# Performance work log

Measured on AMD Instinct MI355X. Metric: run time of the kernel, lower is better.

The kernel has to match this reference:

```python
import jax, jax.numpy as jnp
import numpy as np

MASK_NUM = float(-2**32 + 1)  # additive masking constant from the original module


def setup_inputs() -> dict:
    key = jax.random.key(0)
    kq, kk, kv, km = jax.random.split(key, 4)
    BH, S, D = 32, 2048, 64   # batch*heads, seq_len, head_dim
    B = 4                     # true batch (masks leading dim)
    queries = jax.random.normal(kq, (BH, S, D), dtype=jnp.float32)
    keys = jax.random.normal(kk, (BH, S, D), dtype=jnp.float32)
    values = jax.random.normal(kv, (BH, S, D), dtype=jnp.float32)
    masks = jax.random.randint(km, (B, S), 0, 2, dtype=jnp.int32)  # 1 = masked key
    return {"queries": queries, "keys": keys, "values": values, "masks": masks}


def reference(queries, keys, values, masks):
    d = queries.shape[-1]
    # QK^T, scaled by sqrt(d): [BH, Sq, Sk]
    scores = jnp.einsum('bqd,bkd->bqk', queries, keys) / (d ** 0.5)
    # key-padding mask: tile [B, Sk] -> [BH, Sk], additive large negative
    heads = queries.shape[0] // masks.shape[0]
    m = jnp.tile(masks.astype(jnp.float32), (heads, 1))[:, None, :]  # [BH,1,Sk]
    scores = scores + m * MASK_NUM
    # causal (future) mask: replace upper-triangular entries with MASK_NUM
    Sq, Sk = scores.shape[1], scores.shape[2]
    tril = jnp.tril(jnp.ones((Sq, Sk), dtype=scores.dtype))
    scores = jnp.where(tril == 0, MASK_NUM, scores)
    attn = jax.nn.softmax(scores, axis=-1)
    # dropout_rate = 0.0 -> identity
    return jnp.einsum('bqk,bkd->bqd', attn, values)
```

## Files before the change

kernel.cpp:

```cpp
#include <hip/hip_runtime.h>
#include <hip/hip_bf16.h>

#define S_LEN  2048
#define DHEAD  64
#define NHEADS 32
#define NBATCH 4
#define LOG2E  1.44269504f
#define CMASK  (-4294967296.0f * 1.44269504f)
#define MFIX   16.0f

typedef __attribute__((ext_vector_type(4)))  float f4;
typedef __attribute__((ext_vector_type(8)))  short bh8;
typedef __attribute__((ext_vector_type(16))) float f16x;
typedef __attribute__((ext_vector_type(4)))  int   i4;
typedef __attribute__((ext_vector_type(2)))  int   i2;
typedef unsigned short ushort_t;

static __device__ __forceinline__ unsigned short f2b(float f){
    unsigned int x = __builtin_bit_cast(unsigned int, f);
    x += 0x7FFFu + ((x >> 16) & 1u);
    return (unsigned short)(x >> 16);
}
static __device__ __forceinline__ float b2f(ushort_t u){
    return __builtin_bit_cast(float, ((unsigned)u) << 16);
}
static __device__ __forceinline__ int cvtpk(float a, float b){
    int r; asm("v_cvt_pk_bf16_f32 %0, %1, %2" : "=v"(r) : "v"(a), "v"(b)); return r;
}

__global__ __launch_bounds__(256)
void prep(const float* __restrict__ K, const float* __restrict__ V,
          const int* __restrict__ M,
          ushort_t* __restrict__ Kb, ushort_t* __restrict__ Vt,
          float* __restrict__ colpart, unsigned* __restrict__ mbits)
{
    const int bid = blockIdx.x;
    const int tid = threadIdx.x;
    if (bid < 2048){
        const int i = bid * 256 + tid;
        const f4* p = (const f4*)(K + (size_t)i * 8);
        f4 a = p[0], b = p[1];
        bh8 w;
        #pragma unroll
        for (int k = 0; k < 4; ++k){ w[k] = (short)f2b(a[k]); w[k+4] = (short)f2b(b[k]); }
        *(bh8*)(Kb + (size_t)i * 8) = w;
    } else if (bid < 3072){
        __shared__ short T[64][72];
        __shared__ float red[64][4];
        const int r2 = bid - 2048;
        const int head = r2 >> 5;
        const int kv0  = (r2 & 31) * 64;
        {
            const int r = tid >> 2;
            const int s = (tid & 3) * 16;
            const float* vp = V + ((size_t)head * S_LEN + kv0 + r) * DHEAD + s;
            f4 v0 = *(const f4*)(vp);
            f4 v1 = *(const f4*)(vp + 4);
            f4 v2 = *(const f4*)(vp + 8);
            f4 v3 = *(const f4*)(vp + 12);
            float vv[16];
            *(f4*)&vv[0] = v0; *(f4*)&vv[4] = v1; *(f4*)&vv[8] = v2; *(f4*)&vv[12] = v3;
            #pragma unroll
            for (int i = 0; i < 16; ++i) T[r][s + i] = (short)f2b(vv[i]);
        }
        __syncthreads();
        {
            const int d  = tid >> 2;
            const int k0 = (tid & 3) * 16;
            bh8 w0, w1;
            float s16 = 0.f;
            #pragma unroll
            for (int i = 0; i < 8; ++i){
                w0[i] = T[k0 + i][d];
                w1[i] = T[k0 + 8 + i][d];
                s16 += b2f((ushort_t)w0[i]) + b2f((ushort_t)w1[i]);
            }
            ushort_t* op = Vt + ((size_t)head * DHEAD + d) * S_LEN + kv0 + k0;
            *(bh8*)op       = w0;
            *(bh8*)(op + 8) = w1;
            red[d][tid & 3] = s16;
        }
        __syncthreads();
        if (tid < 64)
            colpart[(size_t)r2 * 64 + tid] =
                red[tid][0] + red[tid][1] + red[tid][2] + red[tid][3];
    } else {
        const int* mp = M + ((size_t)(tid >> 6) << 11) + ((tid & 63) << 5);
        unsigned bits = 0u;
        #pragma unroll
        for (int j = 0; j < 32; j += 4){
            i4 v = *(const i4*)(mp + j);
            bits |= (v[0] != 0 ? (1u << j) : 0u) | (v[1] != 0 ? (2u << j) : 0u)
                  | (v[2] != 0 ? (4u << j) : 0u) | (v[3] != 0 ? (8u << j) : 0u);
        }
        mbits[tid] = bits;
    }
}

__global__ __launch_bounds__(256, 2)
void attn_main(const float* __restrict__ Q, const ushort_t* __restrict__ Kb,
               const ushort_t* __restrict__ Vt, const unsigned* __restrict__ mbits,
               ushort_t* __restrict__ Obuf, float* __restrict__ lbuf)
{
    __shared__ char SMEM[2][16384];

    const int tid  = threadIdx.x;
    const int wave = tid >> 6;
    const int lane = tid & 63;
    const int lq   = lane & 31;
    const int hi   = lane >> 5;

    const int bid  = blockIdx.x;
    const int head = ((bid & 7) << 2) | ((bid >> 3) & 3);
    const int c    = bid >> 5;
    const int s    = c & 1;
    const int j    = 15 - (c >> 1);
    const int b    = head & (NBATCH - 1);
    const size_t hoff = (size_t)head * S_LEN * DHEAD;

    const int q0w = (j << 7) + (wave << 5);
    const int dq  = q0w + lq;
    const int td  = q0w >> 6;
    const int kt0 = s * (j + 1);
    const int ntb = j + 1;

    const ushort_t* kbase = Kb + hoff;
    const ushort_t* vbase = Vt + (size_t)head * DHEAD * S_LEN;

    const int mwords = __builtin_bit_cast(int, mbits[(b << 6) + lane]);

    bh8 qB[4];
    {
        const float* qp = Q + hoff + (size_t)(q0w + lq) * DHEAD;
        const float qs = 0.125f * LOG2E;
        #pragma unroll
        for (int ks = 0; ks < 4; ++ks){
            f4 f0 = *(const f4*)(qp + ks * 16 + hi * 8);
            f4 f1 = *(const f4*)(qp + ks * 16 + hi * 8 + 4);
            bh8 aa;
            #pragma unroll
            for (int i = 0; i < 4; ++i){
                aa[i]   = (short)f2b(f0[i] * qs);
                aa[i+4] = (short)f2b(f1[i] * qs);
            }
            qB[ks] = aa;
        }
    }

    auto stage = [&](int buf, int kv0){
        #pragma unroll
        for (int i = 0; i < 2; ++i){
            const int o   = ((i << 8) + tid) << 4;
            const int row = o >> 7;
            const int cb  = (o & 127) ^ ((row & 7) << 4);
            const char* ks = (const char*)kbase + (size_t)(kv0 + row) * 128 + cb;
            const char* vs = (const char*)vbase + (size_t)row * (S_LEN * 2)
                             + (size_t)kv0 * 2 + cb;
            __builtin_amdgcn_global_load_lds(
                (const __attribute__((address_space(1))) void*)ks,
                (__attribute__((address_space(3))) void*)(&SMEM[buf][o]), 16, 0, 0);
            __builtin_amdgcn_global_load_lds(
                (const __attribute__((address_space(1))) void*)vs,
                (__attribute__((address_space(3))) void*)(&SMEM[buf][8192 + o]), 16, 0, 0);
        }
    };

    f16x acc0 = {};
    f16x acc1 = {};
    float l = 0.f;

    stage(0, kt0 << 6);
    asm volatile("s_waitcnt vmcnt(0)" ::: "memory");
    __syncthreads();

    for (int i = 0; i < ntb; ++i){
        const int cur = i & 1;
        const int kt  = kt0 + i;
        if (i + 1 < ntb) stage(cur ^ 1, (kt + 1) << 6);

        if (kt <= td){
            const int kv0 = kt << 6;
            const char* kb = &SMEM[cur][0];
            const char* vb = &SMEM[cur][8192];

            bh8 kf[8];
            #pragma unroll
            for (int t32 = 0; t32 < 2; ++t32)
                #pragma unroll
                for (int ks = 0; ks < 4; ++ks){
                    const int rl = (t32 << 5) + lq;
                    const int cb = ((ks << 5) + (hi << 4)) ^ ((rl & 7) << 4);
                    kf[t32*4+ks] = *(const bh8*)(kb + (rl << 7) + cb);
                }

            f16x s0, s1;
            #pragma unroll
            for (int i2_ = 0; i2_ < 16; ++i2_){ s0[i2_] = -MFIX; s1[i2_] = -MFIX; }
            __builtin_amdgcn_s_setprio(1);
            #pragma unroll
            for (int ks = 0; ks < 4; ++ks)
                s0 = __builtin_amdgcn_mfma_f32_32x32x16_bf16(kf[ks],   qB[ks], s0, 0, 0, 0);
            #pragma unroll
            for (int ks = 0; ks < 4; ++ks)
                s1 = __builtin_amdgcn_mfma_f32_32x32x16_bf16(kf[4+ks], qB[ks], s1, 0, 0, 0);
            __builtin_amdgcn_s_setprio(0);

            bh8 vf[8];
            #pragma unroll
            for (int aa = 0; aa < 2; ++aa)
                #pragma unroll
                for (int j4 = 0; j4 < 4; ++j4){
                    const int rl = (aa << 5) + lq;
                    const int cb = ((j4 << 5) + (hi << 4)) ^ ((rl & 7) << 4);
                    vf[aa*4+j4] = *(const bh8*)(vb + (rl << 7) + cb);
                }

            const unsigned ml0 = ((unsigned)__builtin_amdgcn_readlane(mwords, 2*kt    )) >> (hi << 2);
            const unsigned ml1 = ((unsigned)__builtin_amdgcn_readlane(mwords, 2*kt + 1)) >> (hi << 2);
            #pragma unroll
            for (int g = 0; g < 4; ++g)
                #pragma unroll
                for (int i2_ = 0; i2_ < 4; ++i2_){
                    s0[g*4+i2_] = ((ml0 >> (g*8+i2_)) & 1u) ? CMASK : s0[g*4+i2_];
                    s1[g*4+i2_] = ((ml1 >> (g*8+i2_)) & 1u) ? CMASK : s1[g*4+i2_];
                }
            if (kt == td){
                #pragma unroll
                for (int g = 0; g < 4; ++g)
                    #pragma unroll
                    for (int i2_ = 0; i2_ < 4; ++i2_){
                        const int k0i = kv0 + (g << 3) + (hi << 2) + i2_;
                        s0[g*4+i2_] = (k0i      > dq) ? CMASK : s0[g*4+i2_];
                        s1[g*4+i2_] = (k0i + 32 > dq) ? CMASK : s1[g*4+i2_];
                    }
            }

            #pragma unroll
            for (int i2_ = 0; i2_ < 16; ++i2_){
                s0[i2_] = __builtin_amdgcn_exp2f(s0[i2_]);
                s1[i2_] = __builtin_amdgcn_exp2f(s1[i2_]);
            }
            float u8[8];
            #pragma unroll
            for (int i2_ = 0; i2_ < 8; ++i2_) u8[i2_] = (s0[i2_] + s0[i2_+8]) + (s1[i2_] + s1[i2_+8]);
            #pragma unroll
            for (int i2_ = 0; i2_ < 4; ++i2_) u8[i2_] = u8[i2_] + u8[i2_+4];
            float lsl = (u8[0] + u8[1]) + (u8[2] + u8[3]);
            l += lsl + __shfl_xor(lsl, 32, 64);

            bh8 pa[4];
            #pragma unroll
            for (int half = 0; half < 2; ++half){
                const f16x& sv = half ? s1 : s0;
                int D[8];
                #pragma unroll
                for (int g = 0; g < 4; ++g){
                    D[2*g]   = cvtpk(sv[4*g],   sv[4*g+1]);
                    D[2*g+1] = cvtpk(sv[4*g+2], sv[4*g+3]);
                }
                int sA0 = hi ? D[0] : D[2],  sA1 = hi ? D[1] : D[3];
                int sB0 = hi ? D[4] : D[6],  sB1 = hi ? D[5] : D[7];
                int rA0 = __shfl_xor(sA0, 32, 64), rA1 = __shfl_xor(sA1, 32, 64);
                int rB0 = __shfl_xor(sB0, 32, 64), rB1 = __shfl_xor(sB1, 32, 64);
                i4 p0 = { hi ? rA0 : D[0], hi ? rA1 : D[1],
                          hi ? D[2] : rA0, hi ? D[3] : rA1 };
                i4 p1 = { hi ? rB0 : D[4], hi ? rB1 : D[5],
                          hi ? D[6] : rB0, hi ? D[7] : rB1 };
                pa[half*2]     = __builtin_bit_cast(bh8, p0);
                pa[half*2 + 1] = __builtin_bit_cast(bh8, p1);
            }

            __builtin_amdgcn_s_setprio(1);
            #pragma unroll
            for (int j4 = 0; j4 < 4; ++j4){
                acc0 = __builtin_amdgcn_mfma_f32_32x32x16_bf16(vf[j4],   pa[j4], acc0, 0, 0, 0);
                acc1 = __builtin_amdgcn_mfma_f32_32x32x16_bf16(vf[4+j4], pa[j4], acc1, 0, 0, 0);
            }
            __builtin_amdgcn_s_setprio(0);
        }

        asm volatile("s_waitcnt vmcnt(0)" ::: "memory");
        __syncthreads();
    }

    ushort_t* ob = Obuf + (((size_t)(s * NHEADS + head) * S_LEN + q0w + lq) << 6);
    #pragma unroll
    for (int g = 0; g < 4; ++g){
        i2 w0, w1;
        w0[0] = cvtpk(acc0[4*g],   acc0[4*g+1]);
        w0[1] = cvtpk(acc0[4*g+2], acc0[4*g+3]);
        w1[0] = cvtpk(acc1[4*g],   acc1[4*g+1]);
        w1[1] = cvtpk(acc1[4*g+2], acc1[4*g+3]);
        *(i2*)((char*)ob + 16*g + 8*hi)      = w0;
        *(i2*)((char*)ob + 64 + 16*g + 8*hi) = w1;
    }
    if (hi == 0)
        lbuf[(size_t)(s * NHEADS + head) * S_LEN + q0w + lq] = l;
}

__global__ __launch_bounds__(256)
void attn_merge(const ushort_t* __restrict__ Obuf, const float* __restrict__ lbuf,
                float* __restrict__ Out)
{
    const int gid  = blockIdx.x * 256 + threadIdx.x;
    const int row  = gid >> 2;
    const int part = gid & 3;
    const float l0 = lbuf[row];
    const float l1 = lbuf[(size_t)(NHEADS * S_LEN) + row];
    const float inv = 1.0f / (l0 + l1);
    const ushort_t* o0 = Obuf + ((size_t)row << 6) + part * 16;
    const ushort_t* o1 = o0 + ((size_t)(NHEADS * S_LEN) << 6);
    bh8 x0a = *(const bh8*)(o0), x0b = *(const bh8*)(o0 + 8);
    bh8 x1a = *(const bh8*)(o1), x1b = *(const bh8*)(o1 + 8);
    float* op = Out + ((size_t)row << 6) + part * 16;
    #pragma unroll
    for (int i = 0; i < 8; ++i){
        op[i]     = (b2f((ushort_t)x0a[i]) + b2f((ushort_t)x1a[i])) * inv;
        op[8 + i] = (b2f((ushort_t)x0b[i]) + b2f((ushort_t)x1b[i])) * inv;
    }
}

__global__ __launch_bounds__(256)
void attn_fixup(const float* __restrict__ colpart, const int* __restrict__ M,
                float* __restrict__ Out)
{
    __shared__ float red[4][64];
    __shared__ int qstar;
    const int head = blockIdx.x;
    const int b = head & (NBATCH - 1);
    const int tid = threadIdx.x;
    const int col = tid & 63;
    const int grp = tid >> 6;
    {
        float s = 0.f;
        const float* cp = colpart + ((size_t)head * 32 + grp * 8) * 64 + col;
        #pragma unroll
        for (int j = 0; j < 8; ++j) s += cp[j * 64];
        red[grp][col] = s;
    }
    if (tid == 0){
        int q = 0;
        const int* mp = M + (size_t)b * S_LEN;
        while (q < S_LEN && mp[q]) ++q;
        qstar = q;
    }
    __syncthreads();
    const int qs = qstar;
    if (qs == 0) return;
    const float mean = (red[0][col] + red[1][col] + red[2][col] + red[3][col])
                       * (1.0f / S_LEN);
    for (int q = grp; q < qs; q += 4)
        Out[((size_t)head * S_LEN + q) * DHEAD + col] = mean;
}

extern "C" void kernel_launch(void* const* d_in, const int* in_sizes, int n_in,
                              void* d_out, int out_size, void* d_ws, size_t ws_size,
                              hipStream_t stream)
{
    const float* Q = (const float*)d_in[0];
    const float* K = (const float*)d_in[1];
    const float* V = (const float*)d_in[2];
    const int*   M = (const int*)d_in[3];
    float* Out = (float*)d_out;

    ushort_t* Kb = (ushort_t*)d_ws;
    ushort_t* Vt = Kb + (size_t)NHEADS * S_LEN * DHEAD;
    float* colpart = (float*)(Vt + (size_t)NHEADS * S_LEN * DHEAD);
    unsigned* mbits = (unsigned*)(colpart + 1024 * 64);
    ushort_t* Obuf = (ushort_t*)(mbits + 256);
    float* lbuf = (float*)(Obuf + ((size_t)2 * NHEADS * S_LEN * DHEAD));

    prep      <<<dim3(3073),   dim3(256), 0, stream>>>(K, V, M, Kb, Vt, colpart, mbits);
    attn_main <<<dim3(1024),   dim3(256), 0, stream>>>(Q, Kb, Vt, mbits, Obuf, lbuf);
    attn_merge<<<dim3(1024),   dim3(256), 0, stream>>>(Obuf, lbuf, Out);
    attn_fixup<<<dim3(NHEADS), dim3(256), 0, stream>>>(colpart, M, Out);
}
```

Measured before the change: 61.17 us.

## Software-pipeline QK^T of next tile ahead of softmax/PV of current tile

Splits the loop body into a QK^T stage and a softmax+PV stage. The QK^T MFMAs for tile i+1 now run right after the barrier, while softmax and PV for tile i run in the next iteration, using two ping-pong score register sets. The aim is to overlap MFMA work with exp/convert/shuffle VALU work and hide the LDS/barrier latency. The cost is higher VGPR pressure from holding two extra 32-float score sets, which could reduce occupancy or cause spills.

```diff
diff --git a/kernel.cpp b/kernel.cpp
--- a/kernel.cpp
+++ b/kernel.cpp
@@ -169,118 +169,131 @@
     f16x acc1 = {};
     float l = 0.f;
 
+    auto qk = [&](int cur, int kt, f16x& o0, f16x& o1){
+        if (kt > td) return;
+        const char* kb = &SMEM[cur][0];
+        bh8 kf[8];
+        #pragma unroll
+        for (int t32 = 0; t32 < 2; ++t32)
+            #pragma unroll
+            for (int ks = 0; ks < 4; ++ks){
+                const int rl = (t32 << 5) + lq;
+                const int cb = ((ks << 5) + (hi << 4)) ^ ((rl & 7) << 4);
+                kf[t32*4+ks] = *(const bh8*)(kb + (rl << 7) + cb);
+            }
+        #pragma unroll
+        for (int i2_ = 0; i2_ < 16; ++i2_){ o0[i2_] = -MFIX; o1[i2_] = -MFIX; }
+        __builtin_amdgcn_s_setprio(1);
+        #pragma unroll
+        for (int ks = 0; ks < 4; ++ks)
+            o0 = __builtin_amdgcn_mfma_f32_32x32x16_bf16(kf[ks],   qB[ks], o0, 0, 0, 0);
+        #pragma unroll
+        for (int ks = 0; ks < 4; ++ks)
+            o1 = __builtin_amdgcn_mfma_f32_32x32x16_bf16(kf[4+ks], qB[ks], o1, 0, 0, 0);
+        __builtin_amdgcn_s_setprio(0);
+    };
+
+    auto softPV = [&](int cur, int kt, f16x& s0v, f16x& s1v){
+        if (kt > td) return;
+        const int kv0 = kt << 6;
+        const char* vb = &SMEM[cur][8192];
+
+        bh8 vf[8];
+        #pragma unroll
+        for (int aa = 0; aa < 2; ++aa)
+            #pragma unroll
+            for (int j4 = 0; j4 < 4; ++j4){
+                const int rl = (aa << 5) + lq;
+                const int cb = ((j4 << 5) + (hi << 4)) ^ ((rl & 7) << 4);
+                vf[aa*4+j4] = *(const bh8*)(vb + (rl << 7) + cb);
+            }
+
+        const unsigned ml0 = ((unsigned)__builtin_amdgcn_readlane(mwords, 2*kt    )) >> (hi << 2);
+        const unsigned ml1 = ((unsigned)__builtin_amdgcn_readlane(mwords, 2*kt + 1)) >> (hi << 2);
+        #pragma unroll
+        for (int g = 0; g < 4; ++g)
+            #pragma unroll
+            for (int i2_ = 0; i2_ < 4; ++i2_){
+                s0v[g*4+i2_] = ((ml0 >> (g*8+i2_)) & 1u) ? CMASK : s0v[g*4+i2_];
+                s1v[g*4+i2_] = ((ml1 >> (g*8+i2_)) & 1u) ? CMASK : s1v[g*4+i2_];
+            }
+        if (kt == td){
+            #pragma unroll
+            for (int g = 0; g < 4; ++g)
+                #pragma unroll
+                for (int i2_ = 0; i2_ < 4; ++i2_){
+                    const int k0i = kv0 + (g << 3) + (hi << 2) + i2_;
+                    s0v[g*4+i2_] = (k0i      > dq) ? CMASK : s0v[g*4+i2_];
+                    s1v[g*4+i2_] = (k0i + 32 > dq) ? CMASK : s1v[g*4+i2_];
+                }
+        }
+
+        #pragma unroll
+        for (int i2_ = 0; i2_ < 16; ++i2_){
+            s0v[i2_] = __builtin_amdgcn_exp2f(s0v[i2_]);
+            s1v[i2_] = __builtin_amdgcn_exp2f(s1v[i2_]);
+        }
+        float u8[8];
+        #pragma unroll
+        for (int i2_ = 0; i2_ < 8; ++i2_) u8[i2_] = (s0v[i2_] + s0v[i2_+8]) + (s1v[i2_] + s1v[i2_+8]);
+        #pragma unroll
+        for (int i2_ = 0; i2_ < 4; ++i2_) u8[i2_] = u8[i2_] + u8[i2_+4];
+        float lsl = (u8[0] + u8[1]) + (u8[2] + u8[3]);
+        l += lsl + __shfl_xor(lsl, 32, 64);
+
+        bh8 pa[4];
+        #pragma unroll
+        for (int half = 0; half < 2; ++half){
+            const f16x& sv = half ? s1v : s0v;
+            int D[8];
+            #pragma unroll
+            for (int g = 0; g < 4; ++g){
+                D[2*g]   = cvtpk(sv[4*g],   sv[4*g+1]);
+                D[2*g+1] = cvtpk(sv[4*g+2], sv[4*g+3]);
+            }
+            int sA0 = hi ? D[0] : D[2],  sA1 = hi ? D[1] : D[3];
+            int sB0 = hi ? D[4] : D[6],  sB1 = hi ? D[5] : D[7];
+            int rA0 = __shfl_xor(sA0, 32, 64), rA1 = __shfl_xor(sA1, 32, 64);
+            int rB0 = __shfl_xor(sB0, 32, 64), rB1 = __shfl_xor(sB1, 32, 64);
+            i4 p0 = { hi ? rA0 : D[0], hi ? rA1 : D[1],
+                      hi ? D[2] : rA0, hi ? D[3] : rA1 };
+            i4 p1 = { hi ? rB0 : D[4], hi ? rB1 : D[5],
+                      hi ? D[6] : rB0, hi ? D[7] : rB1 };
+            pa[half*2]     = __builtin_bit_cast(bh8, p0);
+            pa[half*2 + 1] = __builtin_bit_cast(bh8, p1);
+        }
+
+        __builtin_amdgcn_s_setprio(1);
+        #pragma unroll
+        for (int j4 = 0; j4 < 4; ++j4){
+            acc0 = __builtin_amdgcn_mfma_f32_32x32x16_bf16(vf[j4],   pa[j4], acc0, 0, 0, 0);
+            acc1 = __builtin_amdgcn_mfma_f32_32x32x16_bf16(vf[4+j4], pa[j4], acc1, 0, 0, 0);
+        }
+        __builtin_amdgcn_s_setprio(0);
+    };
+
+    f16x sA0, sA1, sB0, sB1;
+
     stage(0, kt0 << 6);
     asm volatile("s_waitcnt vmcnt(0)" ::: "memory");
     __syncthreads();
-
-    for (int i = 0; i < ntb; ++i){
+    qk(0, kt0, sA0, sA1);
+
+    for (int i = 0; i < ntb - 1; ++i){
         const int cur = i & 1;
         const int kt  = kt0 + i;
-        if (i + 1 < ntb) stage(cur ^ 1, (kt + 1) << 6);
-
-        if (kt <= td){
-            const int kv0 = kt << 6;
-            const char* kb = &SMEM[cur][0];
-            const char* vb = &SMEM[cur][8192];
-
-            bh8 kf[8];
-            #pragma unroll
-            for (int t32 = 0; t32 < 2; ++t32)
-                #pragma unroll
-                for (int ks = 0; ks < 4; ++ks){
-                    const int rl = (t32 << 5) + lq;
-                    const int cb = ((ks << 5) + (hi << 4)) ^ ((rl & 7) << 4);
-                    kf[t32*4+ks] = *(const bh8*)(kb + (rl << 7) + cb);
-                }
-
-            f16x s0, s1;
-            #pragma unroll
-            for (int i2_ = 0; i2_ < 16; ++i2_){ s0[i2_] = -MFIX; s1[i2_] = -MFIX; }
-            __builtin_amdgcn_s_setprio(1);
-            #pragma unroll
-            for (int ks = 0; ks < 4; ++ks)
-                s0 = __builtin_amdgcn_mfma_f32_32x32x16_bf16(kf[ks],   qB[ks], s0, 0, 0, 0);
-            #pragma unroll
-            for (int ks = 0; ks < 4; ++ks)
-                s1 = __builtin_amdgcn_mfma_f32_32x32x16_bf16(kf[4+ks], qB[ks], s1, 0, 0, 0);
-            __builtin_amdgcn_s_setprio(0);
-
-            bh8 vf[8];
-            #pragma unroll
-            for (int aa = 0; aa < 2; ++aa)
-                #pragma unroll
-                for (int j4 = 0; j4 < 4; ++j4){
-                    const int rl = (aa << 5) + lq;
-                    const int cb = ((j4 << 5) + (hi << 4)) ^ ((rl & 7) << 4);
-                    vf[aa*4+j4] = *(const bh8*)(vb + (rl << 7) + cb);
-                }
-
-            const unsigned ml0 = ((unsigned)__builtin_amdgcn_readlane(mwords, 2*kt    )) >> (hi << 2);
-            const unsigned ml1 = ((unsigned)__builtin_amdgcn_readlane(mwords, 2*kt + 1)) >> (hi << 2);
-            #pragma unroll
-            for (int g = 0; g < 4; ++g)
-                #pragma unroll
-                for (int i2_ = 0; i2_ < 4; ++i2_){
-                    s0[g*4+i2_] = ((ml0 >> (g*8+i2_)) & 1u) ? CMASK : s0[g*4+i2_];
-                    s1[g*4+i2_] = ((ml1 >> (g*8+i2_)) & 1u) ? CMASK : s1[g*4+i2_];
-                }
-            if (kt == td){
-                #pragma unroll
-                for (int g = 0; g < 4; ++g)
-                    #pragma unroll
-                    for (int i2_ = 0; i2_ < 4; ++i2_){
-                        const int k0i = kv0 + (g << 3) + (hi << 2) + i2_;
-                        s0[g*4+i2_] = (k0i      > dq) ? CMASK : s0[g*4+i2_];
-                        s1[g*4+i2_] = (k0i + 32 > dq) ? CMASK : s1[g*4+i2_];
-                    }
-            }
-
-            #pragma unroll
-            for (int i2_ = 0; i2_ < 16; ++i2_){
-                s0[i2_] = __builtin_amdgcn_exp2f(s0[i2_]);
-                s1[i2_] = __builtin_amdgcn_exp2f(s1[i2_]);
-            }
-            float u8[8];
-            #pragma unroll
-            for (int i2_ = 0; i2_ < 8; ++i2_) u8[i2_] = (s0[i2_] + s0[i2_+8]) + (s1[i2_] + s1[i2_+8]);
-            #pragma unroll
-            for (int i2_ = 0; i2_ < 4; ++i2_) u8[i2_] = u8[i2_] + u8[i2_+4];
-            float lsl = (u8[0] + u8[1]) + (u8[2] + u8[3]);
-            l += lsl + __shfl_xor(lsl, 32, 64);
-
-            bh8 pa[4];
-            #pragma unroll
-            for (int half = 0; half < 2; ++half){
-                const f16x& sv = half ? s1 : s0;
-                int D[8];
-                #pragma unroll
-                for (int g = 0; g < 4; ++g){
-                    D[2*g]   = cvtpk(sv[4*g],   sv[4*g+1]);
-                    D[2*g+1] = cvtpk(sv[4*g+2], sv[4*g+3]);
-                }
-                int sA0 = hi ? D[0] : D[2],  sA1 = hi ? D[1] : D[3];
-                int sB0 = hi ? D[4] : D[6],  sB1 = hi ? D[5] : D[7];
-                int rA0 = __shfl_xor(sA0, 32, 64), rA1 = __shfl_xor(sA1, 32, 64);
-                int rB0 = __shfl_xor(sB0, 32, 64), rB1 = __shfl_xor(sB1, 32, 64);
-                i4 p0 = { hi ? rA0 : D[0], hi ? rA1 : D[1],
-                          hi ? D[2] : rA0, hi ? D[3] : rA1 };
-                i4 p1 = { hi ? rB0 : D[4], hi ? rB1 : D[5],
-                          hi ? D[6] : rB0, hi ? D[7] : rB1 };
-                pa[half*2]     = __builtin_bit_cast(bh8, p0);
-                pa[half*2 + 1] = __builtin_bit_cast(bh8, p1);
-            }
-
-            __builtin_amdgcn_s_setprio(1);
-            #pragma unroll
-            for (int j4 = 0; j4 < 4; ++j4){
-                acc0 = __builtin_amdgcn_mfma_f32_32x32x16_bf16(vf[j4],   pa[j4], acc0, 0, 0, 0);
-                acc1 = __builtin_amdgcn_mfma_f32_32x32x16_bf16(vf[4+j4], pa[j4], acc1, 0, 0, 0);
-            }
-            __builtin_amdgcn_s_setprio(0);
-        }
-
+        stage(cur ^ 1, (kt + 1) << 6);
+        if (i & 1) softPV(cur, kt, sB0, sB1);
+        else       softPV(cur, kt, sA0, sA1);
         asm volatile("s_waitcnt vmcnt(0)" ::: "memory");
         __syncthreads();
+        if (i & 1) qk(cur ^ 1, kt + 1, sA0, sA1);
+        else       qk(cur ^ 1, kt + 1, sB0, sB1);
+    }
+    {
+        const int i = ntb - 1, cur = i & 1, kt = kt0 + i;
+        if (i & 1) softPV(cur, kt, sB0, sB1);
+        else       softPV(cur, kt, sA0, sA1);
     }
 
     ushort_t* ob = Obuf + (((size_t)(s * NHEADS + head) * S_LEN + q0w + lq) << 6);
```

Measured after the change: 69.10 us. +13.0%, slower.
